# Kernel optimization log

Hardware: AMD Instinct MI355X
Metric: run time of the kernel (lower is better)

The kernel has to match this reference:

```python
import jax, jax.numpy as jnp
import numpy as np

ELEM, EMBD, WIN = 128, 128, 128

def setup_inputs() -> dict:
    key = jax.random.key(0)
    ks = jax.random.split(key, 7)
    s = 1.0 / np.sqrt(ELEM)
    return {
        "x": jax.random.normal(ks[0], (8, 16384, ELEM), dtype=jnp.float32),
        "Wq": jax.random.uniform(ks[1], (EMBD, ELEM), jnp.float32, -s, s),
        "bq": jax.random.uniform(ks[2], (EMBD,), jnp.float32, -s, s),
        "Wk": jax.random.uniform(ks[3], (EMBD, ELEM), jnp.float32, -s, s),
        "bk": jax.random.uniform(ks[4], (EMBD,), jnp.float32, -s, s),
        "Wv": jax.random.uniform(ks[5], (EMBD, ELEM), jnp.float32, -s, s),
        "bv": jax.random.uniform(ks[6], (EMBD,), jnp.float32, -s, s),
    }

def reference(x, Wq, bq, Wk, bk, Wv, bv):
    N, S, E = x.shape
    P = S // WIN
    xp = x.reshape(N, P, WIN, E)  # [N,P,W,E]
    q = jnp.einsum('npwe,de->npwd', xp, Wq) + bq
    k = jnp.einsum('npwe,de->npwd', xp, Wk) + bk
    v = jnp.einsum('npwe,de->npwd', xp, Wv) + bv
    # note: original applies NO 1/sqrt(d) scaling
    scores = jnp.einsum('npwd,npud->npwu', q, k)  # [N,P,W,W]
    attn = jax.nn.softmax(scores, axis=-1)
    out = jnp.einsum('npwu,npud->npwd', attn, v)
    return out.reshape(N, S, EMBD)
```

## Files before the change

### kernel.cpp

```cpp
#include <hip/hip_runtime.h>

#define LDSP 136

typedef _Float16 h8 __attribute__((ext_vector_type(8)));
typedef _Float16 h4 __attribute__((ext_vector_type(4)));
typedef float    f4 __attribute__((ext_vector_type(4)));

__global__ void prep_mt(const float* __restrict__ Wq, const float* __restrict__ Wk,
                        _Float16* __restrict__ Mt) {
    int idx = blockIdx.x * 256 + threadIdx.x;
    int e = idx & 127, f = idx >> 7;
    float acc = 0.f;
    for (int d = 0; d < 128; ++d)
        acc += Wk[d * 128 + f] * Wq[d * 128 + e];
    Mt[idx] = (_Float16)acc;
}

__global__ void prep_rest(const float* __restrict__ Wv, const float* __restrict__ Wk,
                          const float* __restrict__ bq, _Float16* __restrict__ Wvh,
                          float* __restrict__ ck) {
    int t = threadIdx.x;
    for (int i = 0; i < 16; ++i) {
        int off = (t + i * 256) * 4;
        f4 f = *(const f4*)(Wv + off);
        h4 h = {(_Float16)f.x, (_Float16)f.y, (_Float16)f.z, (_Float16)f.w};
        *(h4*)(Wvh + off) = h;
    }
    if (t < 128) {
        float acc = 0.f;
        for (int d = 0; d < 128; ++d) acc += bq[d] * Wk[d * 128 + t];
        ck[t] = acc;
    }
}

__global__ __launch_bounds__(512, 2) void attn(
    const float* __restrict__ x, const _Float16* __restrict__ Mt,
    const _Float16* __restrict__ Wvh, const float* __restrict__ ck,
    const float* __restrict__ bv, float* __restrict__ out) {
    __shared__ _Float16 Xs[2][128 * LDSP];
    __shared__ _Float16 Ts[128 * LDSP];
    __shared__ _Float16 Vs[128 * LDSP];

    const int tid  = threadIdx.x;
    const int wave = tid >> 6;
    const int lane = tid & 63;
    const int quad = lane >> 4;
    const int l16  = lane & 15;
    const int wb   = wave * 16;

    h8 aT[4], aV[4];
    for (int e0 = 0; e0 < 4; ++e0) {
        aT[e0] = *(const h8*)(Mt  + (wb + l16) * 128 + e0 * 32 + quad * 8);
        aV[e0] = *(const h8*)(Wvh + (wb + l16) * 128 + e0 * 32 + quad * 8);
    }
    f4 ck4  = *(const f4*)(ck + wb + quad * 4);
    float bvv = bv[wb + l16];

    const size_t base0 = (size_t)blockIdx.x * 4 * (128 * 128);

    f4 pf[8];
    for (int j = 0; j < 8; ++j)
        pf[j] = *(const f4*)(x + base0 + 4 * tid + 2048 * j);

    for (int it = 0; it < 4; ++it) {
        _Float16* X = Xs[it & 1];

        for (int j = 0; j < 8; ++j) {
            int idx = 4 * tid + 2048 * j;
            int row = idx >> 7, col = idx & 127;
            f4 f = pf[j];
            h4 h = {(_Float16)f.x, (_Float16)f.y, (_Float16)f.z, (_Float16)f.w};
            *(h4*)(&X[row * LDSP + col]) = h;
        }
        __syncthreads();

        if (it < 3) {
            const float* nx = x + base0 + (size_t)(it + 1) * (128 * 128);
            for (int j = 0; j < 8; ++j)
                pf[j] = *(const f4*)(nx + 4 * tid + 2048 * j);
        }

        {
            f4 accT[8], accV[8];
            for (int t = 0; t < 8; ++t) {
                accT[t] = ck4;
                accV[t] = (f4){bvv, bvv, bvv, bvv};
            }
            for (int e0 = 0; e0 < 4; ++e0) {
                h8 b[8];
                for (int nt = 0; nt < 8; ++nt)
                    b[nt] = *(const h8*)(&X[(nt * 16 + l16) * LDSP + e0 * 32 + quad * 8]);
                for (int nt = 0; nt < 8; ++nt) {
                    accT[nt] = __builtin_amdgcn_mfma_f32_16x16x32_f16(aT[e0], b[nt], accT[nt], 0, 0, 0);
                    accV[nt] = __builtin_amdgcn_mfma_f32_16x16x32_f16(b[nt], aV[e0], accV[nt], 0, 0, 0);
                }
            }
            for (int nt = 0; nt < 8; ++nt) {
                f4 v = accT[nt];
                h4 h = {(_Float16)v.x, (_Float16)v.y, (_Float16)v.z, (_Float16)v.w};
                *(h4*)(&Ts[(nt * 16 + l16) * LDSP + wb + quad * 4]) = h;
                v = accV[nt];
                h4 g = {(_Float16)v.x, (_Float16)v.y, (_Float16)v.z, (_Float16)v.w};
                *(h4*)(&Vs[(wb + l16) * LDSP + nt * 16 + quad * 4]) = g;
            }
        }
        __syncthreads();

        f4 acc[8];
        for (int mt = 0; mt < 8; ++mt) acc[mt] = (f4){0.f, 0.f, 0.f, 0.f};
        for (int f0 = 0; f0 < 4; ++f0) {
            h8 bt = *(const h8*)(&Ts[(wb + l16) * LDSP + f0 * 32 + quad * 8]);
            h8 a[8];
            for (int mt = 0; mt < 8; ++mt)
                a[mt] = *(const h8*)(&X[(mt * 16 + l16) * LDSP + f0 * 32 + quad * 8]);
            for (int mt = 0; mt < 8; ++mt)
                acc[mt] = __builtin_amdgcn_mfma_f32_16x16x32_f16(a[mt], bt, acc[mt], 0, 0, 0);
        }
        {
            float m = -1e30f;
            for (int mt = 0; mt < 8; ++mt) {
                f4 v = acc[mt];
                m = fmaxf(m, fmaxf(fmaxf(v.x, v.y), fmaxf(v.z, v.w)));
            }
            m = fmaxf(m, __shfl_xor(m, 16, 64));
            m = fmaxf(m, __shfl_xor(m, 32, 64));
            float s = 0.f;
            for (int mt = 0; mt < 8; ++mt) {
                f4 v = acc[mt];
                v.x = __expf(v.x - m); v.y = __expf(v.y - m);
                v.z = __expf(v.z - m); v.w = __expf(v.w - m);
                acc[mt] = v;
                s += v.x + v.y + v.z + v.w;
            }
            s += __shfl_xor(s, 16, 64);
            s += __shfl_xor(s, 32, 64);
            float inv = 1.0f / s;
            for (int mt = 0; mt < 8; ++mt) {
                f4 v = acc[mt];
                h4 h = {(_Float16)(v.x * inv), (_Float16)(v.y * inv),
                        (_Float16)(v.z * inv), (_Float16)(v.w * inv)};
                *(h4*)(&Ts[(wb + l16) * LDSP + mt * 16 + quad * 4]) = h;
            }
        }

        for (int nt = 0; nt < 8; ++nt) acc[nt] = (f4){0.f, 0.f, 0.f, 0.f};
        for (int u0 = 0; u0 < 4; ++u0) {
            h8 ap = *(const h8*)(&Ts[(wb + l16) * LDSP + u0 * 32 + quad * 8]);
            h8 b[8];
            for (int nt = 0; nt < 8; ++nt)
                b[nt] = *(const h8*)(&Vs[(nt * 16 + l16) * LDSP + u0 * 32 + quad * 8]);
            for (int nt = 0; nt < 8; ++nt)
                acc[nt] = __builtin_amdgcn_mfma_f32_16x16x32_f16(ap, b[nt], acc[nt], 0, 0, 0);
        }
        float* ob = out + base0 + (size_t)it * (128 * 128);
        for (int nt = 0; nt < 8; ++nt) {
            f4 v = acc[nt];
            int w0 = wb + quad * 4;
            int d  = nt * 16 + l16;
            ob[(size_t)(w0 + 0) * 128 + d] = v.x;
            ob[(size_t)(w0 + 1) * 128 + d] = v.y;
            ob[(size_t)(w0 + 2) * 128 + d] = v.z;
            ob[(size_t)(w0 + 3) * 128 + d] = v.w;
        }
    }
}

extern "C" void kernel_launch(void* const* d_in, const int* in_sizes, int n_in,
                              void* d_out, int out_size, void* d_ws, size_t ws_size,
                              hipStream_t stream) {
    const float* x  = (const float*)d_in[0];
    const float* Wq = (const float*)d_in[1];
    const float* bq = (const float*)d_in[2];
    const float* Wk = (const float*)d_in[3];
    const float* Wv = (const float*)d_in[5];
    const float* bv = (const float*)d_in[6];

    _Float16* Mt  = (_Float16*)d_ws;
    _Float16* Wvh = Mt + 16384;
    float*    ckp = (float*)(Wvh + 16384);

    prep_mt<<<64, 256, 0, stream>>>(Wq, Wk, Mt);
    prep_rest<<<1, 256, 0, stream>>>(Wv, Wk, bq, Wvh, ckp);
    attn<<<256, 512, 0, stream>>>(x, Mt, Wvh, ckp, bv, (float*)d_out);
}
```

Measured before the change: 142.5 us.

## Rewrite attention kernel with 32x32 MFMA tiles, XOR-swizzled LDS, fused prep kernel

```diff
diff --git a/kernel.cpp b/kernel.cpp
--- a/kernel.cpp
+++ b/kernel.cpp
@@ -1,35 +1,43 @@
 #include <hip/hip_runtime.h>
-
-#define LDSP 136
 
 typedef _Float16 h8 __attribute__((ext_vector_type(8)));
 typedef _Float16 h4 __attribute__((ext_vector_type(4)));
 typedef float    f4 __attribute__((ext_vector_type(4)));
-
-__global__ void prep_mt(const float* __restrict__ Wq, const float* __restrict__ Wk,
-                        _Float16* __restrict__ Mt) {
-    int idx = blockIdx.x * 256 + threadIdx.x;
-    int e = idx & 127, f = idx >> 7;
-    float acc = 0.f;
-    for (int d = 0; d < 128; ++d)
-        acc += Wk[d * 128 + f] * Wq[d * 128 + e];
-    Mt[idx] = (_Float16)acc;
-}
-
-__global__ void prep_rest(const float* __restrict__ Wv, const float* __restrict__ Wk,
-                          const float* __restrict__ bq, _Float16* __restrict__ Wvh,
-                          float* __restrict__ ck) {
-    int t = threadIdx.x;
-    for (int i = 0; i < 16; ++i) {
-        int off = (t + i * 256) * 4;
-        f4 f = *(const f4*)(Wv + off);
-        h4 h = {(_Float16)f.x, (_Float16)f.y, (_Float16)f.z, (_Float16)f.w};
-        *(h4*)(Wvh + off) = h;
-    }
-    if (t < 128) {
+typedef float    f16v __attribute__((ext_vector_type(16)));
+
+__device__ __forceinline__ int sw(int row, int col) {
+    return row * 128 + ((((col >> 3) ^ (row & 15)) << 3) | (col & 7));
+}
+
+__device__ __forceinline__ f16v zero16() {
+    f16v z;
+    for (int i = 0; i < 16; ++i) z[i] = 0.f;
+    return z;
+}
+
+__global__ void prep(const float* __restrict__ Wq, const float* __restrict__ Wk,
+                     const float* __restrict__ Wv, const float* __restrict__ bq,
+                     _Float16* __restrict__ Mt, _Float16* __restrict__ Wvh,
+                     float* __restrict__ ck) {
+    if (blockIdx.x < 64) {
+        int idx = blockIdx.x * 256 + threadIdx.x;
+        int e = idx & 127, f = idx >> 7;
         float acc = 0.f;
-        for (int d = 0; d < 128; ++d) acc += bq[d] * Wk[d * 128 + t];
-        ck[t] = acc;
+        for (int d = 0; d < 128; ++d) acc += Wk[d * 128 + f] * Wq[d * 128 + e];
+        Mt[idx] = (_Float16)acc;
+    } else {
+        int t = threadIdx.x;
+        for (int i = 0; i < 16; ++i) {
+            int off = (t + i * 256) * 4;
+            f4 f = *(const f4*)(Wv + off);
+            h4 h = {(_Float16)f.x, (_Float16)f.y, (_Float16)f.z, (_Float16)f.w};
+            *(h4*)(Wvh + off) = h;
+        }
+        if (t < 128) {
+            float a = 0.f;
+            for (int d = 0; d < 128; ++d) a += bq[d] * Wk[d * 128 + t];
+            ck[t] = a;
+        }
     }
 }
 
@@ -37,27 +45,34 @@
     const float* __restrict__ x, const _Float16* __restrict__ Mt,
     const _Float16* __restrict__ Wvh, const float* __restrict__ ck,
     const float* __restrict__ bv, float* __restrict__ out) {
-    __shared__ _Float16 Xs[2][128 * LDSP];
-    __shared__ _Float16 Ts[128 * LDSP];
-    __shared__ _Float16 Vs[128 * LDSP];
+    __shared__ __attribute__((aligned(16))) _Float16 Xs[2][16384];
+    __shared__ __attribute__((aligned(16))) _Float16 Ts[16384];
+    __shared__ __attribute__((aligned(16))) _Float16 Vs[16384];
+    __shared__ __attribute__((aligned(16))) float ckL[128];
+    __shared__ __attribute__((aligned(16))) float redM[2][128];
+    __shared__ __attribute__((aligned(16))) float redS[2][128];
 
     const int tid  = threadIdx.x;
-    const int wave = tid >> 6;
+    const int wv   = tid >> 6;
     const int lane = tid & 63;
-    const int quad = lane >> 4;
-    const int l16  = lane & 15;
-    const int wb   = wave * 16;
-
-    h8 aT[4], aV[4];
-    for (int e0 = 0; e0 < 4; ++e0) {
-        aT[e0] = *(const h8*)(Mt  + (wb + l16) * 128 + e0 * 32 + quad * 8);
-        aV[e0] = *(const h8*)(Wvh + (wb + l16) * 128 + e0 * 32 + quad * 8);
+    const int l32  = lane & 31;
+    const int half = lane >> 5;
+    const int b    = wv & 3;
+    const int h    = wv >> 2;
+
+    if (tid < 128) ckL[tid] = ck[tid];
+
+    h8 mtA[2][8], wvB[2][8];
+    for (int fi = 0; fi < 2; ++fi) {
+        int F = 2 * h + fi;
+        for (int k0 = 0; k0 < 8; ++k0) {
+            mtA[fi][k0] = *(const h8*)(Mt  + (F * 32 + l32) * 128 + k0 * 16 + half * 8);
+            wvB[fi][k0] = *(const h8*)(Wvh + (F * 32 + l32) * 128 + k0 * 16 + half * 8);
+        }
     }
-    f4 ck4  = *(const f4*)(ck + wb + quad * 4);
-    float bvv = bv[wb + l16];
-
-    const size_t base0 = (size_t)blockIdx.x * 4 * (128 * 128);
-
+    float bvv[2] = { bv[(2 * h + 0) * 32 + l32], bv[(2 * h + 1) * 32 + l32] };
+
+    const size_t base0 = (size_t)blockIdx.x * 4 * 16384;
     f4 pf[8];
     for (int j = 0; j < 8; ++j)
         pf[j] = *(const f4*)(x + base0 + 4 * tid + 2048 * j);
@@ -69,98 +84,125 @@
             int idx = 4 * tid + 2048 * j;
             int row = idx >> 7, col = idx & 127;
             f4 f = pf[j];
-            h4 h = {(_Float16)f.x, (_Float16)f.y, (_Float16)f.z, (_Float16)f.w};
-            *(h4*)(&X[row * LDSP + col]) = h;
+            h4 hv = {(_Float16)f.x, (_Float16)f.y, (_Float16)f.z, (_Float16)f.w};
+            *(h4*)(&X[sw(row, col)]) = hv;
         }
         __syncthreads();
 
         if (it < 3) {
-            const float* nx = x + base0 + (size_t)(it + 1) * (128 * 128);
+            const float* nx = x + base0 + (size_t)(it + 1) * 16384;
             for (int j = 0; j < 8; ++j)
                 pf[j] = *(const f4*)(nx + 4 * tid + 2048 * j);
         }
 
-        {
-            f4 accT[8], accV[8];
-            for (int t = 0; t < 8; ++t) {
-                accT[t] = ck4;
-                accV[t] = (f4){bvv, bvv, bvv, bvv};
-            }
-            for (int e0 = 0; e0 < 4; ++e0) {
-                h8 b[8];
-                for (int nt = 0; nt < 8; ++nt)
-                    b[nt] = *(const h8*)(&X[(nt * 16 + l16) * LDSP + e0 * 32 + quad * 8]);
-                for (int nt = 0; nt < 8; ++nt) {
-                    accT[nt] = __builtin_amdgcn_mfma_f32_16x16x32_f16(aT[e0], b[nt], accT[nt], 0, 0, 0);
-                    accV[nt] = __builtin_amdgcn_mfma_f32_16x16x32_f16(b[nt], aV[e0], accV[nt], 0, 0, 0);
+        const int xr = b * 32 + l32;
+
+        {
+            f16v a0 = zero16(), a1 = zero16();
+            for (int k0 = 0; k0 < 8; ++k0) {
+                h8 xf = *(const h8*)(&X[xr * 128 + (((k0 * 2 + half) ^ (xr & 15)) << 3)]);
+                a0 = __builtin_amdgcn_mfma_f32_32x32x16_f16(mtA[0][k0], xf, a0, 0, 0, 0);
+                a1 = __builtin_amdgcn_mfma_f32_32x32x16_f16(mtA[1][k0], xf, a1, 0, 0, 0);
+            }
+            int w = xr;
+            for (int fi = 0; fi < 2; ++fi) {
+                int F = 2 * h + fi;
+                f16v a = fi ? a1 : a0;
+                for (int q = 0; q < 4; ++q) {
+                    f4 cb = *(const f4*)(&ckL[F * 32 + q * 8 + 4 * half]);
+                    h4 hv = {(_Float16)(a[4 * q + 0] + cb.x), (_Float16)(a[4 * q + 1] + cb.y),
+                             (_Float16)(a[4 * q + 2] + cb.z), (_Float16)(a[4 * q + 3] + cb.w)};
+                    *(h4*)(&Ts[w * 128 + (((F * 4 + q) ^ (w & 15)) << 3) + 4 * half]) = hv;
                 }
             }
-            for (int nt = 0; nt < 8; ++nt) {
-                f4 v = accT[nt];
-                h4 h = {(_Float16)v.x, (_Float16)v.y, (_Float16)v.z, (_Float16)v.w};
-                *(h4*)(&Ts[(nt * 16 + l16) * LDSP + wb + quad * 4]) = h;
-                v = accV[nt];
-                h4 g = {(_Float16)v.x, (_Float16)v.y, (_Float16)v.z, (_Float16)v.w};
-                *(h4*)(&Vs[(wb + l16) * LDSP + nt * 16 + quad * 4]) = g;
-            }
-        }
-        __syncthreads();
-
-        f4 acc[8];
-        for (int mt = 0; mt < 8; ++mt) acc[mt] = (f4){0.f, 0.f, 0.f, 0.f};
-        for (int f0 = 0; f0 < 4; ++f0) {
-            h8 bt = *(const h8*)(&Ts[(wb + l16) * LDSP + f0 * 32 + quad * 8]);
-            h8 a[8];
-            for (int mt = 0; mt < 8; ++mt)
-                a[mt] = *(const h8*)(&X[(mt * 16 + l16) * LDSP + f0 * 32 + quad * 8]);
-            for (int mt = 0; mt < 8; ++mt)
-                acc[mt] = __builtin_amdgcn_mfma_f32_16x16x32_f16(a[mt], bt, acc[mt], 0, 0, 0);
-        }
-        {
-            float m = -1e30f;
-            for (int mt = 0; mt < 8; ++mt) {
-                f4 v = acc[mt];
-                m = fmaxf(m, fmaxf(fmaxf(v.x, v.y), fmaxf(v.z, v.w)));
-            }
-            m = fmaxf(m, __shfl_xor(m, 16, 64));
+        }
+        {
+            f16v a0 = zero16(), a1 = zero16();
+            for (int k0 = 0; k0 < 8; ++k0) {
+                h8 xf = *(const h8*)(&X[xr * 128 + (((k0 * 2 + half) ^ (xr & 15)) << 3)]);
+                a0 = __builtin_amdgcn_mfma_f32_32x32x16_f16(xf, wvB[0][k0], a0, 0, 0, 0);
+                a1 = __builtin_amdgcn_mfma_f32_32x32x16_f16(xf, wvB[1][k0], a1, 0, 0, 0);
+            }
+            for (int di = 0; di < 2; ++di) {
+                int d = (2 * h + di) * 32 + l32;
+                f16v a = di ? a1 : a0;
+                for (int q = 0; q < 4; ++q) {
+                    h4 hv = {(_Float16)(a[4 * q + 0] + bvv[di]), (_Float16)(a[4 * q + 1] + bvv[di]),
+                             (_Float16)(a[4 * q + 2] + bvv[di]), (_Float16)(a[4 * q + 3] + bvv[di])};
+                    *(h4*)(&Vs[d * 128 + (((b * 4 + q) ^ (d & 15)) << 3) + 4 * half]) = hv;
+                }
+            }
+        }
+        __syncthreads();
+
+        f16v s0 = zero16(), s1 = zero16();
+        {
+            int r0 = (2 * h + 0) * 32 + l32, r1 = (2 * h + 1) * 32 + l32;
+            for (int k0 = 0; k0 < 8; ++k0) {
+                h8 tf = *(const h8*)(&Ts[xr * 128 + (((k0 * 2 + half) ^ (xr & 15)) << 3)]);
+                h8 x0 = *(const h8*)(&X[r0 * 128 + (((k0 * 2 + half) ^ (r0 & 15)) << 3)]);
+                h8 x1 = *(const h8*)(&X[r1 * 128 + (((k0 * 2 + half) ^ (r1 & 15)) << 3)]);
+                s0 = __builtin_amdgcn_mfma_f32_32x32x16_f16(x0, tf, s0, 0, 0, 0);
+                s1 = __builtin_amdgcn_mfma_f32_32x32x16_f16(x1, tf, s1, 0, 0, 0);
+            }
+        }
+        {
+            float m = s0[0];
+            for (int r = 1; r < 16; ++r) m = fmaxf(m, s0[r]);
+            for (int r = 0; r < 16; ++r) m = fmaxf(m, s1[r]);
             m = fmaxf(m, __shfl_xor(m, 32, 64));
-            float s = 0.f;
-            for (int mt = 0; mt < 8; ++mt) {
-                f4 v = acc[mt];
-                v.x = __expf(v.x - m); v.y = __expf(v.y - m);
-                v.z = __expf(v.z - m); v.w = __expf(v.w - m);
-                acc[mt] = v;
-                s += v.x + v.y + v.z + v.w;
-            }
-            s += __shfl_xor(s, 16, 64);
-            s += __shfl_xor(s, 32, 64);
-            float inv = 1.0f / s;
-            for (int mt = 0; mt < 8; ++mt) {
-                f4 v = acc[mt];
-                h4 h = {(_Float16)(v.x * inv), (_Float16)(v.y * inv),
-                        (_Float16)(v.z * inv), (_Float16)(v.w * inv)};
-                *(h4*)(&Ts[(wb + l16) * LDSP + mt * 16 + quad * 4]) = h;
-            }
-        }
-
-        for (int nt = 0; nt < 8; ++nt) acc[nt] = (f4){0.f, 0.f, 0.f, 0.f};
-        for (int u0 = 0; u0 < 4; ++u0) {
-            h8 ap = *(const h8*)(&Ts[(wb + l16) * LDSP + u0 * 32 + quad * 8]);
-            h8 b[8];
-            for (int nt = 0; nt < 8; ++nt)
-                b[nt] = *(const h8*)(&Vs[(nt * 16 + l16) * LDSP + u0 * 32 + quad * 8]);
-            for (int nt = 0; nt < 8; ++nt)
-                acc[nt] = __builtin_amdgcn_mfma_f32_16x16x32_f16(ap, b[nt], acc[nt], 0, 0, 0);
-        }
-        float* ob = out + base0 + (size_t)it * (128 * 128);
-        for (int nt = 0; nt < 8; ++nt) {
-            f4 v = acc[nt];
-            int w0 = wb + quad * 4;
-            int d  = nt * 16 + l16;
-            ob[(size_t)(w0 + 0) * 128 + d] = v.x;
-            ob[(size_t)(w0 + 1) * 128 + d] = v.y;
-            ob[(size_t)(w0 + 2) * 128 + d] = v.z;
-            ob[(size_t)(w0 + 3) * 128 + d] = v.w;
+            if (lane < 32) redM[h][b * 32 + lane] = m;
+        }
+        __syncthreads();
+
+        const int w = b * 32 + l32;
+        {
+            float M = fmaxf(redM[0][w], redM[1][w]);
+            float sum = 0.f;
+            _Float16* Ps = X;
+            for (int t = 0; t < 2; ++t) {
+                f16v s = t ? s1 : s0;
+                int mb = 2 * h + t;
+                for (int q = 0; q < 4; ++q) {
+                    float e0 = __expf(s[4 * q + 0] - M), e1 = __expf(s[4 * q + 1] - M);
+                    float e2 = __expf(s[4 * q + 2] - M), e3 = __expf(s[4 * q + 3] - M);
+                    sum += e0 + e1 + e2 + e3;
+                    h4 hv = {(_Float16)e0, (_Float16)e1, (_Float16)e2, (_Float16)e3};
+                    *(h4*)(&Ps[w * 128 + (((mb * 4 + q) ^ (w & 15)) << 3) + 4 * half]) = hv;
+                }
+            }
+            sum += __shfl_xor(sum, 32, 64);
+            if (lane < 32) redS[h][b * 32 + lane] = sum;
+        }
+        __syncthreads();
+
+        f16v o0 = zero16(), o1 = zero16();
+        {
+            const _Float16* Ps = X;
+            int d0r = (2 * h + 0) * 32 + l32, d1r = (2 * h + 1) * 32 + l32;
+            for (int k0 = 0; k0 < 8; ++k0) {
+                h8 pfr = *(const h8*)(&Ps[w * 128 + (((k0 * 2 + half) ^ (w & 15)) << 3)]);
+                h8 v0 = *(const h8*)(&Vs[d0r * 128 + (((k0 * 2 + half) ^ (d0r & 15)) << 3)]);
+                h8 v1 = *(const h8*)(&Vs[d1r * 128 + (((k0 * 2 + half) ^ (d1r & 15)) << 3)]);
+                o0 = __builtin_amdgcn_mfma_f32_32x32x16_f16(pfr, v0, o0, 0, 0, 0);
+                o1 = __builtin_amdgcn_mfma_f32_32x32x16_f16(pfr, v1, o1, 0, 0, 0);
+            }
+        }
+        float* ob = out + base0 + (size_t)it * 16384;
+        for (int q = 0; q < 4; ++q) {
+            int wr = b * 32 + q * 8 + 4 * half;
+            f4 z0 = *(const f4*)(&redS[0][wr]);
+            f4 z1 = *(const f4*)(&redS[1][wr]);
+            f4 inv = {1.f / (z0.x + z1.x), 1.f / (z0.y + z1.y),
+                      1.f / (z0.z + z1.z), 1.f / (z0.w + z1.w)};
+            for (int di = 0; di < 2; ++di) {
+                f16v a = di ? o1 : o0;
+                int d = (2 * h + di) * 32 + l32;
+                ob[(size_t)(wr + 0) * 128 + d] = a[4 * q + 0] * inv.x;
+                ob[(size_t)(wr + 1) * 128 + d] = a[4 * q + 1] * inv.y;
+                ob[(size_t)(wr + 2) * 128 + d] = a[4 * q + 2] * inv.z;
+                ob[(size_t)(wr + 3) * 128 + d] = a[4 * q + 3] * inv.w;
+            }
         }
     }
 }
@@ -179,7 +221,6 @@
     _Float16* Wvh = Mt + 16384;
     float*    ckp = (float*)(Wvh + 16384);
 
-    prep_mt<<<64, 256, 0, stream>>>(Wq, Wk, Mt);
-    prep_rest<<<1, 256, 0, stream>>>(Wv, Wk, bq, Wvh, ckp);
+    prep<<<65, 256, 0, stream>>>(Wq, Wk, Wv, bq, Mt, Wvh, ckp);
     attn<<<256, 512, 0, stream>>>(x, Mt, Wvh, ckp, bv, (float*)d_out);
 }
```

Result: slower. 193.1 us (+35.5%).
